# Kernel tuning notes

Measured on AMD Instinct MI355X. Metric: run time of the kernel, lower is better.

The kernel has to match this reference:

```python
import jax, jax.numpy as jnp
import numpy as np

D = 1024      # in/out token dims
E = 2048      # expanded dim = 2*D
S_ATT = 128   # attention feature dim s
EPS = 1e-5
SQRT_S = np.sqrt(S_ATT).astype(np.float32)


def setup_inputs() -> dict:
    key = jax.random.key(0)
    ks = jax.random.split(key, 8)
    B, S = 4, 2048
    x = jax.random.normal(ks[0], (B, S, D), dtype=jnp.float32)
    pos_enc = jax.random.normal(ks[1], (S, S_ATT), dtype=jnp.float32)
    # uv Linear: xavier_uniform on weight of shape [2e+s, D]
    fan_out = 2 * E + S_ATT
    limit = np.sqrt(6.0 / (D + fan_out)).astype(np.float32)
    uv_w = jax.random.uniform(ks[2], (fan_out, D), dtype=jnp.float32, minval=-limit, maxval=limit)
    # o Linear: default kaiming-uniform-ish; plain uniform works for a reference
    lim_o = np.sqrt(1.0 / E).astype(np.float32)
    o_w = jax.random.uniform(ks[3], (D, E), dtype=jnp.float32, minval=-lim_o, maxval=lim_o)
    gamma = jax.random.uniform(ks[4], (2, S_ATT), dtype=jnp.float32)
    beta = jax.random.uniform(ks[5], (2, S_ATT), dtype=jnp.float32)
    ln_g = jnp.ones((), dtype=jnp.float32)          # ScaleNorm learnable scalar
    res_scale = jnp.ones((D,), dtype=jnp.float32)   # ChannelWiseScale
    return {"x": x, "pos_enc": pos_enc, "uv_w": uv_w, "o_w": o_w,
            "gamma": gamma, "beta": beta, "ln_g": ln_g, "res_scale": res_scale}


def _gau(x, pos_enc, uv_w, o_w, gamma, beta, ln_g, res_scale):
    # ScaleNorm: x / max(||x|| * d^-0.5, eps) * g
    norm = jnp.linalg.norm(x, axis=-1, keepdims=True) * (D ** -0.5)
    xn = x / jnp.maximum(norm, EPS) * ln_g
    uv = jax.nn.silu(jnp.einsum('bsd,fd->bsf', xn, uv_w))  # [B,S,2E+s]
    u, v, base = uv[..., :E], uv[..., E:2 * E], uv[..., 2 * E:]
    # per-head affine: base[...,None,:]*gamma+beta -> q,k
    qk_base = base[..., None, :] * gamma + beta             # [B,S,2,s]
    q = qk_base[..., 0, :] + pos_enc[None, :, :]            # 'add' pos enc
    k = qk_base[..., 1, :] + pos_enc[None, :, :]
    scores = jnp.einsum('bqs,bks->bqk', q, k) / SQRT_S
    kernel = jnp.square(jax.nn.relu(scores))                # squared-ReLU attention
    attn_v = jnp.einsum('bqk,bke->bqe', kernel, v)
    out = jnp.einsum('bqe,de->bqd', u * attn_v, o_w)
    # residual shortcut with channel-wise scale (in == out dims)
    return x * res_scale + out


def reference(x, pos_enc, uv_w, o_w, gamma, beta, ln_g, res_scale):
    return _gau(x, pos_enc, uv_w, o_w, gamma, beta, ln_g, res_scale)
```

## Files before the change

### kernel.cpp

```cpp
#include <hip/hip_runtime.h>

typedef unsigned short u16;
typedef __bf16 bf16x8 __attribute__((ext_vector_type(8)));
typedef float f32x4 __attribute__((ext_vector_type(4)));

#define SEQ   2048
#define DDIM  1024
#define EDIM  2048
#define FDIM  4224
#define FPAD  4352
#define SATT  128
#define NBATCH 4

__device__ __forceinline__ u16 f2bf(float f) {
  unsigned u = __float_as_uint(f);
  unsigned r = (u + 0x7fffu + ((u >> 16) & 1u)) >> 16;
  return (u16)r;
}
__device__ __forceinline__ float bf2f(u16 v) {
  return __uint_as_float(((unsigned)v) << 16);
}

__device__ __forceinline__ void gload16(const u16* g, u16* l) {
  auto gp = (const __attribute__((address_space(1))) u16*)(unsigned long long)g;
  auto lp = (__attribute__((address_space(3))) u16*)(unsigned)(unsigned long long)l;
  __builtin_amdgcn_global_load_lds(gp, lp, 16, 0, 0);
}


__global__ void cvt_bf16_kernel(const float* __restrict__ in, u16* __restrict__ out, int n4) {
  int i = blockIdx.x * blockDim.x + threadIdx.x;
  if (i >= n4) return;
  float4 v = reinterpret_cast<const float4*>(in)[i];
  unsigned p0 = (unsigned)f2bf(v.x) | ((unsigned)f2bf(v.y) << 16);
  unsigned p1 = (unsigned)f2bf(v.z) | ((unsigned)f2bf(v.w) << 16);
  uint2 pk; pk.x = p0; pk.y = p1;
  reinterpret_cast<uint2*>(out)[i] = pk;
}

__global__ void rms_kernel(const float* __restrict__ x, const float* __restrict__ ln_g,
                           u16* __restrict__ xn) {
  int row = blockIdx.x;
  int t = threadIdx.x;
  const float4* xr = reinterpret_cast<const float4*>(x + (size_t)row * DDIM);
  float4 v = xr[t];
  float s = v.x * v.x + v.y * v.y + v.z * v.z + v.w * v.w;
#pragma unroll
  for (int off = 32; off > 0; off >>= 1) s += __shfl_down(s, off);
  __shared__ float wsum[4];
  int lane = t & 63, wv = t >> 6;
  if (lane == 0) wsum[wv] = s;
  __syncthreads();
  float tot = wsum[0] + wsum[1] + wsum[2] + wsum[3];
  float rms = sqrtf(tot * (1.0f / (float)DDIM));
  float scale = ln_g[0] / fmaxf(rms, 1e-5f);
  unsigned p0 = (unsigned)f2bf(v.x * scale) | ((unsigned)f2bf(v.y * scale) << 16);
  unsigned p1 = (unsigned)f2bf(v.z * scale) | ((unsigned)f2bf(v.w * scale) << 16);
  uint2 pk; pk.x = p0; pk.y = p1;
  reinterpret_cast<uint2*>(xn + (size_t)row * DDIM)[t] = pk;
}

__global__ void qk_kernel(const u16* __restrict__ uv, const float* __restrict__ pos_enc,
                          const float* __restrict__ gamma, const float* __restrict__ beta,
                          u16* __restrict__ q, u16* __restrict__ k, int ldF) {
  int r = blockIdx.x;
  int t = threadIdx.x;
  int s = r & (SEQ - 1);
  float bval = bf2f(uv[(size_t)r * ldF + 2 * EDIM + t]);
  float pe = pos_enc[(size_t)s * SATT + t];
  float qv = bval * gamma[t] + beta[t] + pe;
  float kv = bval * gamma[SATT + t] + beta[SATT + t] + pe;
  q[(size_t)r * SATT + t] = f2bf(qv);
  k[(size_t)r * SATT + t] = f2bf(kv);
}

__global__ void transpose_v(const u16* __restrict__ uv, u16* __restrict__ vt, int ldF) {
  __shared__ u16 tile[32][33];
  int b = blockIdx.z;
  uv += (size_t)b * SEQ * ldF;
  vt += (size_t)b * EDIM * SEQ;
  int e0 = blockIdx.x * 32, s0 = blockIdx.y * 32;
  int tx = threadIdx.x, ty = threadIdx.y;
#pragma unroll
  for (int j = 0; j < 32; j += 8)
    tile[ty + j][tx] = uv[(size_t)(s0 + ty + j) * ldF + EDIM + e0 + tx];
  __syncthreads();
#pragma unroll
  for (int j = 0; j < 32; j += 8)
    vt[(size_t)(e0 + ty + j) * SEQ + s0 + tx] = tile[tx][ty + j];
}

template <int EPI>
__global__ __launch_bounds__(512, 2) void gemm_bt3(
    const u16* __restrict__ A, const u16* __restrict__ B,
    int N, int K,
    u16* __restrict__ Cbf,
    const u16* __restrict__ U, int ldu,
    size_t sA, size_t sB, size_t sC, size_t sU) {
  __shared__ u16 lds[65536];
  const int tid = threadIdx.x;
  const int w = tid >> 6, l = tid & 63;
  const int wm2 = w >> 2, wn2 = w & 3;
  const int fr = l & 15, kg = l >> 4;

  const int bz = blockIdx.z;
  A += (size_t)bz * sA; B += (size_t)bz * sB; U += (size_t)bz * sU;

  const int nbx = gridDim.x;
  int li = blockIdx.y * nbx + blockIdx.x;
  const int cpx = (nbx * gridDim.y) >> 3;
  li = (li & 7) * cpx + (li >> 3);
  const int bn = li % nbx;
  const int bm = li / nbx;

  const int NT = K >> 6;
  const size_t aoff = (size_t)bm * 256 * K;
  const size_t boff = (size_t)bn * 256 * K;

  const int r0 = (w << 3) + (l >> 3);
  const int cswz = (((l & 7) ^ (l >> 3)) & 7) << 3;

  auto stageP = [&](int T, int p) {
    int off = (T & 1) * 65536 + p * 16384;
    const u16* g;
    if (p == 0)      g = A + aoff;
    else if (p == 1) g = A + aoff + (size_t)128 * K;
    else if (p == 2) g = B + boff;
    else             g = B + boff + (size_t)128 * K;
    g += (size_t)r0 * K + (size_t)T * 64 + cswz;
    u16* dst = lds + (off >> 1) + w * 512;
    gload16(g, dst);
    gload16(g + (size_t)64 * K, dst + 4096);
  };

  const char* ldsC = (const char*)lds;
  auto ldA = [&](int buf, int qa, int i, int s) -> bf16x8 {
    int row = wm2 * 64 + i * 16 + fr;
    int off = buf * 65536 + qa * 16384 + row * 128 + s * 64 + kg * 16;
    off ^= (fr & 7) << 4;
    return *(const bf16x8*)(ldsC + off);
  };
  auto ldB = [&](int buf, int qb, int j, int s) -> bf16x8 {
    int row = wn2 * 32 + j * 16 + fr;
    int off = buf * 65536 + 32768 + qb * 16384 + row * 128 + s * 64 + kg * 16;
    off ^= (fr & 7) << 4;
    return *(const bf16x8*)(ldsC + off);
  };

  f32x4 acc[8][4];
#pragma unroll
  for (int i = 0; i < 8; i++)
#pragma unroll
    for (int j = 0; j < 4; j++) acc[i][j] = f32x4{0.f, 0.f, 0.f, 0.f};

  stageP(0, 0); stageP(0, 2); stageP(0, 3); stageP(0, 1);
  if (NT > 1) {
    stageP(1, 0); stageP(1, 2); stageP(1, 3); stageP(1, 1);
    asm volatile("s_waitcnt vmcnt(8)" ::: "memory");
  } else {
    asm volatile("s_waitcnt vmcnt(0)" ::: "memory");
  }
  __builtin_amdgcn_s_barrier();

  bf16x8 aH[4][2], bF[2][2][2];
  for (int t = 0; t < NT; ++t) {
    const int buf = t & 1;
    const bool st = (t + 2 < NT);
#pragma unroll
    for (int i = 0; i < 4; i++)
#pragma unroll
      for (int s = 0; s < 2; s++) aH[i][s] = ldA(buf, 0, i, s);
#pragma unroll
    for (int j = 0; j < 2; j++)
#pragma unroll
      for (int s = 0; s < 2; s++) bF[0][j][s] = ldB(buf, 0, j, s);
    asm volatile("s_waitcnt lgkmcnt(8)" ::: "memory");
    __builtin_amdgcn_s_barrier();
    asm volatile("s_waitcnt lgkmcnt(0)" ::: "memory");
    __builtin_amdgcn_s_setprio(1);
#pragma unroll
    for (int s = 0; s < 2; s++)
#pragma unroll
      for (int i = 0; i < 4; i++)
#pragma unroll
        for (int j = 0; j < 2; j++)
          acc[i][j] = __builtin_amdgcn_mfma_f32_16x16x32_bf16(aH[i][s], bF[0][j][s], acc[i][j], 0, 0, 0);
    __builtin_amdgcn_s_setprio(0);
    __builtin_amdgcn_s_barrier();
#pragma unroll
    for (int j = 0; j < 2; j++)
#pragma unroll
      for (int s = 0; s < 2; s++) bF[1][j][s] = ldB(buf, 1, j, s);
    if (st) { stageP(t + 2, 0); stageP(t + 2, 2); }
    __builtin_amdgcn_s_barrier();
    asm volatile("s_waitcnt lgkmcnt(0)" ::: "memory");
    __builtin_amdgcn_s_setprio(1);
#pragma unroll
    for (int s = 0; s < 2; s++)
#pragma unroll
      for (int i = 0; i < 4; i++)
#pragma unroll
        for (int j = 0; j < 2; j++)
          acc[i][2 + j] = __builtin_amdgcn_mfma_f32_16x16x32_bf16(aH[i][s], bF[1][j][s], acc[i][2 + j], 0, 0, 0);
    __builtin_amdgcn_s_setprio(0);
    __builtin_amdgcn_s_barrier();
#pragma unroll
    for (int i = 0; i < 4; i++)
#pragma unroll
      for (int s = 0; s < 2; s++) aH[i][s] = ldA(buf, 1, i, s);
    if (st) stageP(t + 2, 3);
    __builtin_amdgcn_s_barrier();
    asm volatile("s_waitcnt lgkmcnt(0)" ::: "memory");
    __builtin_amdgcn_s_setprio(1);
#pragma unroll
    for (int s = 0; s < 2; s++)
#pragma unroll
      for (int i = 0; i < 4; i++)
#pragma unroll
        for (int j = 0; j < 2; j++)
          acc[4 + i][j] = __builtin_amdgcn_mfma_f32_16x16x32_bf16(aH[i][s], bF[0][j][s], acc[4 + i][j], 0, 0, 0);
    __builtin_amdgcn_s_setprio(0);
    __builtin_amdgcn_s_barrier();
    if (st) stageP(t + 2, 1);
    __builtin_amdgcn_s_setprio(1);
#pragma unroll
    for (int s = 0; s < 2; s++)
#pragma unroll
      for (int i = 0; i < 4; i++)
#pragma unroll
        for (int j = 0; j < 2; j++)
          acc[4 + i][2 + j] = __builtin_amdgcn_mfma_f32_16x16x32_bf16(aH[i][s], bF[1][j][s], acc[4 + i][2 + j], 0, 0, 0);
    __builtin_amdgcn_s_setprio(0);
    if (st) asm volatile("s_waitcnt vmcnt(6)" ::: "memory");
    else    asm volatile("s_waitcnt vmcnt(0)" ::: "memory");
    __builtin_amdgcn_s_barrier();
  }

  const int rsub = (l >> 4) * 4;
  const int ccol = l & 15;
#pragma unroll
  for (int ai = 0; ai < 8; ai++) {
#pragma unroll
    for (int bj = 0; bj < 4; bj++) {
      int n = bn * 256 + (bj >> 1) * 128 + wn2 * 32 + (bj & 1) * 16 + ccol;
#pragma unroll
      for (int tt = 0; tt < 4; tt++) {
        int m = bm * 256 + (ai >> 2) * 128 + wm2 * 64 + (ai & 3) * 16 + rsub + tt;
        float v = acc[ai][bj][tt];
        size_t idx = (size_t)m * N + n;
        if constexpr (EPI == 0) {
          float sv = v / (1.f + __expf(-v));
          Cbf[(size_t)bz * sC + idx] = f2bf(sv);
        } else if constexpr (EPI == 1) {
          float sc = v * 0.08838834764831845f;
          sc = sc > 0.f ? sc * sc : 0.f;
          Cbf[(size_t)bz * sC + idx] = f2bf(sc);
        } else {
          float uvl = bf2f(U[(size_t)m * ldu + n]);
          Cbf[(size_t)bz * sC + idx] = f2bf(v * uvl);
        }
      }
    }
  }
}

template <int EPI>
__global__ __launch_bounds__(512, 2) void gemm_bt2(
    const u16* __restrict__ A, const u16* __restrict__ B,
    int M, int N, int K,
    u16* __restrict__ Cbf, float* __restrict__ Cf,
    const u16* __restrict__ U, int ldu,
    const float* __restrict__ Xres, const float* __restrict__ rscale,
    size_t sA, size_t sB, size_t sC, size_t sU) {
  __shared__ u16 lds[3 * 24576];
  const int tid = threadIdx.x;
  const int w = tid >> 6, l = tid & 63;
  const int wr = w >> 1, wc = w & 1;
  const int fr = l & 15, kg = l >> 4;

  const int bz = blockIdx.z;
  A += (size_t)bz * sA; B += (size_t)bz * sB; U += (size_t)bz * sU;

  const int nbx = gridDim.x;
  int li = blockIdx.y * nbx + blockIdx.x;
  const int cpx = (nbx * gridDim.y) >> 3;
  li = (li & 7) * cpx + (li >> 3);
  const int bn = li % nbx;
  const int bm = li / nbx;

  const int NT = K >> 6;
  const int srow = (w << 3) + (l >> 3);
  const int scol = (((l & 7) ^ (l >> 3)) & 7) << 3;
  const size_t aoff = (size_t)bm * 256 * K;
  const size_t boff = (size_t)bn * 128 * K;
  const char* ldsC = (const char*)lds;

  auto stageAu = [&](int t, int h) {
    int sb = (t % 3) * 24576 + h * 8192;
    const u16* g = A + aoff + (size_t)(h * 128 + srow) * K + t * 64 + scol;
#pragma unroll
    for (int L = 0; L < 2; L++)
      gload16(g + (size_t)(L * 64) * K, &lds[sb + (L * 8 + w) * 512]);
  };
  auto stageBu = [&](int t) {
    int sb = (t % 3) * 24576 + 16384;
    const u16* g = B + boff + (size_t)srow * K + t * 64 + scol;
#pragma unroll
    for (int L = 0; L < 2; L++)
      gload16(g + (size_t)(L * 64) * K, &lds[sb + (L * 8 + w) * 512]);
  };
  auto ldA = [&](int cur, int i, int s) -> bf16x8 {
    int r = ((wr & 1) << 6) + (i << 4) + fr;
    int off = cur * 49152 + ((wr >> 1) << 14) + (r << 7) + (s << 6) + (kg << 4);
    off ^= (r & 7) << 4;
    return *(const bf16x8*)(ldsC + off);
  };
  auto ldB = [&](int cur, int j, int s) -> bf16x8 {
    int r = (wc << 6) + (j << 4) + fr;
    int off = cur * 49152 + 32768 + (r << 7) + (s << 6) + (kg << 4);
    off ^= (r & 7) << 4;
    return *(const bf16x8*)(ldsC + off);
  };

  f32x4 acc[4][4];
#pragma unroll
  for (int i = 0; i < 4; i++)
#pragma unroll
    for (int j = 0; j < 4; j++) acc[i][j] = f32x4{0.f, 0.f, 0.f, 0.f};

  stageAu(0, 0); stageAu(0, 1); stageBu(0);
  if (NT > 1) { stageAu(1, 0); stageAu(1, 1); stageBu(1); }
  asm volatile("s_waitcnt vmcnt(6)" ::: "memory");
  __builtin_amdgcn_s_barrier();

  bf16x8 aF[2][2], bF[2][2][2];
  for (int t = 0; t < NT; ++t) {
    const int cur = t % 3;
    const bool st = (t + 2 < NT);
#pragma unroll
    for (int i = 0; i < 2; i++)
#pragma unroll
      for (int s = 0; s < 2; s++) aF[i][s] = ldA(cur, i, s);
#pragma unroll
    for (int j = 0; j < 2; j++)
#pragma unroll
      for (int s = 0; s < 2; s++) bF[0][j][s] = ldB(cur, j, s);
    if (st) stageAu(t + 2, 0);
    __builtin_amdgcn_s_barrier();
    __builtin_amdgcn_s_setprio(1);
#pragma unroll
    for (int s = 0; s < 2; s++)
#pragma unroll
      for (int i = 0; i < 2; i++)
#pragma unroll
        for (int j = 0; j < 2; j++)
          acc[i][j] = __builtin_amdgcn_mfma_f32_16x16x32_bf16(aF[i][s], bF[0][j][s], acc[i][j], 0, 0, 0);
    __builtin_amdgcn_s_setprio(0);
    __builtin_amdgcn_s_barrier();
#pragma unroll
    for (int j = 0; j < 2; j++)
#pragma unroll
      for (int s = 0; s < 2; s++) bF[1][j][s] = ldB(cur, 2 + j, s);
    if (st) stageAu(t + 2, 1);
    __builtin_amdgcn_s_barrier();
    __builtin_amdgcn_s_setprio(1);
#pragma unroll
    for (int s = 0; s < 2; s++)
#pragma unroll
      for (int i = 0; i < 2; i++)
#pragma unroll
        for (int j = 0; j < 2; j++)
          acc[i][2 + j] = __builtin_amdgcn_mfma_f32_16x16x32_bf16(aF[i][s], bF[1][j][s], acc[i][2 + j], 0, 0, 0);
    __builtin_amdgcn_s_setprio(0);
    __builtin_amdgcn_s_barrier();
#pragma unroll
    for (int i = 0; i < 2; i++)
#pragma unroll
      for (int s = 0; s < 2; s++) aF[i][s] = ldA(cur, 2 + i, s);
    if (st) stageBu(t + 2);
    __builtin_amdgcn_s_barrier();
    __builtin_amdgcn_s_setprio(1);
#pragma unroll
    for (int s = 0; s < 2; s++)
#pragma unroll
      for (int i = 0; i < 2; i++)
#pragma unroll
        for (int j = 0; j < 2; j++)
          acc[2 + i][j] = __builtin_amdgcn_mfma_f32_16x16x32_bf16(aF[i][s], bF[0][j][s], acc[2 + i][j], 0, 0, 0);
    __builtin_amdgcn_s_setprio(0);
    __builtin_amdgcn_s_barrier();
    __builtin_amdgcn_s_setprio(1);
#pragma unroll
    for (int s = 0; s < 2; s++)
#pragma unroll
      for (int i = 0; i < 2; i++)
#pragma unroll
        for (int j = 0; j < 2; j++)
          acc[2 + i][2 + j] = __builtin_amdgcn_mfma_f32_16x16x32_bf16(aF[i][s], bF[1][j][s], acc[2 + i][2 + j], 0, 0, 0);
    __builtin_amdgcn_s_setprio(0);
    if (st) asm volatile("s_waitcnt vmcnt(6)" ::: "memory");
    else    asm volatile("s_waitcnt vmcnt(0)" ::: "memory");
    __builtin_amdgcn_s_barrier();
  }

  const int m0 = bm * 256 + wr * 64;
  const int n0 = bn * 128 + wc * 64;
  const int rsub = (l >> 4) * 4;
  const int ccol = l & 15;
#pragma unroll
  for (int i = 0; i < 4; i++) {
#pragma unroll
    for (int j = 0; j < 4; j++) {
      int n = n0 + j * 16 + ccol;
#pragma unroll
      for (int tt = 0; tt < 4; tt++) {
        int m = m0 + i * 16 + rsub + tt;
        float v = acc[i][j][tt];
        size_t idx = (size_t)m * N + n;
        if constexpr (EPI == 0) {
          float sv = v / (1.f + __expf(-v));
          Cbf[(size_t)bz * sC + idx] = f2bf(sv);
        } else if constexpr (EPI == 1) {
          float sc = v * 0.08838834764831845f;
          sc = sc > 0.f ? sc * sc : 0.f;
          Cbf[(size_t)bz * sC + idx] = f2bf(sc);
        } else if constexpr (EPI == 2) {
          float uvl = bf2f(U[(size_t)m * ldu + n]);
          Cbf[(size_t)bz * sC + idx] = f2bf(v * uvl);
        } else {
          Cf[idx] = Xres[idx] * rscale[n] + v;
        }
      }
    }
  }
}

template <int EPI>
__global__ __launch_bounds__(256) void gemm_bt(
    const u16* __restrict__ A, const u16* __restrict__ B,
    int M, int N, int K,
    u16* __restrict__ Cbf, float* __restrict__ Cf,
    const u16* __restrict__ U, int ldu,
    const float* __restrict__ Xres, const float* __restrict__ rscale,
    size_t sA, size_t sB, size_t sC, size_t sU) {
  __shared__ u16 As[128 * 32];
  __shared__ u16 Bs[128 * 32];
  const int tid = threadIdx.x;
  const int wave = tid >> 6, lane = tid & 63;
  const int wr = wave >> 1, wc = wave & 1;
  const int bz = blockIdx.z;
  A += (size_t)bz * sA; B += (size_t)bz * sB; U += (size_t)bz * sU;
  const int nbx = gridDim.x;
  int li = blockIdx.y * nbx + blockIdx.x;
  const int cpx = (nbx * gridDim.y) >> 3;
  li = (li & 7) * cpx + (li >> 3);
  const int bn = li % nbx;
  const int bm = li / nbx;
  const size_t abase = (size_t)bm * 128 * K;
  const size_t bbase = (size_t)bn * 128 * K;
  const int srow = tid >> 2;
  const int scol = (tid & 3) * 8;
  f32x4 acc[4][4];
#pragma unroll
  for (int i = 0; i < 4; i++)
#pragma unroll
    for (int j = 0; j < 4; j++) acc[i][j] = f32x4{0.f, 0.f, 0.f, 0.f};
  const int fr = lane & 15;
  const int fk = (lane >> 4) * 8;
  for (int k0 = 0; k0 < K; k0 += 32) {
#pragma unroll
    for (int r = 0; r < 2; r++) {
      const u16* gA = A + abase + (size_t)(r * 64 + srow) * K + k0 + scol;
      const u16* gB = B + bbase + (size_t)(r * 64 + srow) * K + k0 + scol;
      gload16(gA, As + r * 2048 + wave * 512);
      gload16(gB, Bs + r * 2048 + wave * 512);
    }
    __syncthreads();
    bf16x8 af[4], bfr[4];
#pragma unroll
    for (int i = 0; i < 4; i++) {
      af[i]  = *reinterpret_cast<const bf16x8*>(&As[(wr * 64 + i * 16 + fr) * 32 + fk]);
      bfr[i] = *reinterpret_cast<const bf16x8*>(&Bs[(wc * 64 + i * 16 + fr) * 32 + fk]);
    }
#pragma unroll
    for (int i = 0; i < 4; i++)
#pragma unroll
      for (int j = 0; j < 4; j++)
        acc[i][j] = __builtin_amdgcn_mfma_f32_16x16x32_bf16(af[i], bfr[j], acc[i][j], 0, 0, 0);
    __syncthreads();
  }
  const int m0 = bm * 128 + wr * 64;
  const int n0 = bn * 128 + wc * 64;
  const int rsub = (lane >> 4) * 4;
  const int ccol = lane & 15;
#pragma unroll
  for (int i = 0; i < 4; i++) {
#pragma unroll
    for (int j = 0; j < 4; j++) {
      int n = n0 + j * 16 + ccol;
#pragma unroll
      for (int t = 0; t < 4; t++) {
        int m = m0 + i * 16 + rsub + t;
        float v = acc[i][j][t];
        size_t idx = (size_t)m * N + n;
        if constexpr (EPI == 0) {
          float sv = v / (1.f + __expf(-v));
          Cbf[(size_t)bz * sC + idx] = f2bf(sv);
        } else if constexpr (EPI == 1) {
          float sc = v * 0.08838834764831845f;
          sc = sc > 0.f ? sc * sc : 0.f;
          Cbf[(size_t)bz * sC + idx] = f2bf(sc);
        } else if constexpr (EPI == 2) {
          float uvl = bf2f(U[(size_t)m * ldu + n]);
          Cbf[(size_t)bz * sC + idx] = f2bf(v * uvl);
        } else {
          Cf[idx] = Xres[idx] * rscale[n] + v;
        }
      }
    }
  }
}


extern "C" void kernel_launch(void* const* d_in, const int* in_sizes, int n_in,
                              void* d_out, int out_size, void* d_ws, size_t ws_size,
                              hipStream_t stream) {
  const float* x        = (const float*)d_in[0];
  const float* pos_enc  = (const float*)d_in[1];
  const float* uv_w     = (const float*)d_in[2];
  const float* o_w      = (const float*)d_in[3];
  const float* gamma    = (const float*)d_in[4];
  const float* beta     = (const float*)d_in[5];
  const float* ln_g     = (const float*)d_in[6];
  const float* res_scale= (const float*)d_in[7];
  float* out = (float*)d_out;

  auto al = [](size_t b) { return (b + 255) & ~(size_t)255; };
  const size_t SZ_UVWP = (size_t)FPAD * DDIM * 2;
  const size_t SZ_OW   = (size_t)DDIM * EDIM * 2;
  const size_t SZ_Z    = (size_t)NBATCH * SEQ * EDIM * 2;
  const size_t SZ_XN   = (size_t)NBATCH * SEQ * DDIM * 2;
  const size_t SZ_UVP  = (size_t)NBATCH * SEQ * FPAD * 2;
  const size_t SZ_QK   = (size_t)NBATCH * SEQ * SATT * 2;
  const size_t SZ_VT1  = (size_t)EDIM * SEQ * 2;
  const size_t SZ_P1   = (size_t)SEQ * SEQ * 2;
  const size_t need_full =
      al(SZ_UVWP) + al(SZ_OW) + al(SZ_Z) + al(SZ_XN) + al(SZ_UVP) + 2 * al(SZ_QK) +
      (size_t)NBATCH * (al(SZ_VT1) + al(SZ_P1));
  const bool FULL = ws_size >= need_full;

  char* p = (char*)d_ws;
  auto alloc = [&](size_t bytes) {
    char* r = p;
    p += (bytes + 255) & ~(size_t)255;
    return r;
  };

  if (FULL) {
    u16* uvw_bf = (u16*)alloc(SZ_UVWP);
    u16* ow_bf  = (u16*)alloc(SZ_OW);
    u16* z      = (u16*)alloc(SZ_Z);
    u16* vt     = (u16*)alloc((size_t)NBATCH * al(SZ_VT1));
    u16* pmat   = (u16*)alloc((size_t)NBATCH * al(SZ_P1));
    u16* xn     = (u16*)alloc(SZ_XN);
    u16* uv     = (u16*)alloc(SZ_UVP);
    u16* qb     = (u16*)alloc(SZ_QK);
    u16* kb     = (u16*)alloc(SZ_QK);
    const size_t sVT = al(SZ_VT1) >> 1;
    const size_t sP  = al(SZ_P1) >> 1;
    const int rows = NBATCH * SEQ;

    hipMemsetAsync(uvw_bf + (size_t)FDIM * DDIM, 0,
                   (size_t)(FPAD - FDIM) * DDIM * 2, stream);
    cvt_bf16_kernel<<<(FDIM * DDIM / 4 + 255) / 256, 256, 0, stream>>>(
        uv_w, uvw_bf, FDIM * DDIM / 4);
    cvt_bf16_kernel<<<(DDIM * EDIM / 4 + 255) / 256, 256, 0, stream>>>(
        o_w, ow_bf, DDIM * EDIM / 4);

    rms_kernel<<<rows, 256, 0, stream>>>(x, ln_g, xn);
    gemm_bt3<0><<<dim3(FPAD / 256, rows / 256), 512, 0, stream>>>(
        xn, uvw_bf, FPAD, DDIM, uv, nullptr, 0, 0, 0, 0, 0);
    qk_kernel<<<rows, SATT, 0, stream>>>(uv, pos_enc, gamma, beta, qb, kb, FPAD);
    transpose_v<<<dim3(EDIM / 32, SEQ / 32, NBATCH), dim3(32, 8), 0, stream>>>(uv, vt, FPAD);
    gemm_bt3<1><<<dim3(SEQ / 256, SEQ / 256, NBATCH), 512, 0, stream>>>(
        qb, kb, SEQ, SATT, pmat, nullptr, 0,
        (size_t)SEQ * SATT, (size_t)SEQ * SATT, sP, 0);
    gemm_bt3<2><<<dim3(EDIM / 256, SEQ / 256, NBATCH), 512, 0, stream>>>(
        pmat, vt, EDIM, SEQ, z, uv, FPAD,
        sP, sVT, (size_t)SEQ * EDIM, (size_t)SEQ * FPAD);
    gemm_bt2<3><<<dim3(DDIM / 128, rows / 256), 512, 0, stream>>>(
        z, ow_bf, rows, DDIM, EDIM, nullptr, out, nullptr, 0,
        x, res_scale, 0, 0, 0, 0);
    return;
  }

  u16* uvw_bf = (u16*)alloc((size_t)FDIM * DDIM * 2);
  u16* ow_bf  = (u16*)alloc(SZ_OW);
  u16* z      = (u16*)alloc(SZ_Z);
  u16* vt     = (u16*)alloc(SZ_VT1);
  u16* pmat   = (u16*)alloc(SZ_P1);
  size_t fixed = (size_t)(p - (char*)d_ws);
  const size_t perbc = (size_t)SEQ * DDIM * 2 + (size_t)SEQ * FDIM * 2 +
                       2 * (size_t)SEQ * SATT * 2 + 4 * 256;
  int BC = (ws_size >= fixed + 4 * perbc) ? 4 : 1;
  u16* xn = (u16*)alloc((size_t)BC * SEQ * DDIM * 2);
  u16* uv = (u16*)alloc((size_t)BC * SEQ * FDIM * 2);
  u16* qb = (u16*)alloc((size_t)BC * SEQ * SATT * 2);
  u16* kb = (u16*)alloc((size_t)BC * SEQ * SATT * 2);

  cvt_bf16_kernel<<<(FDIM * DDIM / 4 + 255) / 256, 256, 0, stream>>>(
      uv_w, uvw_bf, FDIM * DDIM / 4);
  cvt_bf16_kernel<<<(DDIM * EDIM / 4 + 255) / 256, 256, 0, stream>>>(
      o_w, ow_bf, DDIM * EDIM / 4);

  for (int b0 = 0; b0 < NBATCH; b0 += BC) {
    int rows = BC * SEQ;
    rms_kernel<<<rows, 256, 0, stream>>>(x + (size_t)b0 * SEQ * DDIM, ln_g, xn);
    gemm_bt<0><<<dim3(FDIM / 128, rows / 128), 256, 0, stream>>>(
        xn, uvw_bf, rows, FDIM, DDIM, uv, nullptr, nullptr, 0, nullptr, nullptr,
        0, 0, 0, 0);
    qk_kernel<<<rows, SATT, 0, stream>>>(uv, pos_enc, gamma, beta, qb, kb, FDIM);
    for (int bb = 0; bb < BC; bb++) {
      int b = b0 + bb;
      const u16* uvb = uv + (size_t)bb * SEQ * FDIM;
      transpose_v<<<dim3(EDIM / 32, SEQ / 32, 1), dim3(32, 8), 0, stream>>>(uvb, vt, FDIM);
      gemm_bt<1><<<dim3(SEQ / 128, SEQ / 128), 256, 0, stream>>>(
          qb + (size_t)bb * SEQ * SATT, kb + (size_t)bb * SEQ * SATT,
          SEQ, SEQ, SATT, pmat, nullptr, nullptr, 0, nullptr, nullptr,
          0, 0, 0, 0);
      gemm_bt<2><<<dim3(EDIM / 128, SEQ / 128), 256, 0, stream>>>(
          pmat, vt, SEQ, EDIM, SEQ, z + (size_t)b * SEQ * EDIM, nullptr,
          uvb, FDIM, nullptr, nullptr, 0, 0, 0, 0);
    }
  }
  gemm_bt<3><<<dim3(DDIM / 128, (NBATCH * SEQ) / 128), 256, 0, stream>>>(
      z, ow_bf, NBATCH * SEQ, DDIM, EDIM, nullptr, out, nullptr, 0,
      x, res_scale, 0, 0, 0, 0);
}
```

Measured before the change: 296.1 us.

## Drop FPAD padding with partial-N tile path and precomputed LDS/global pointers

Removes the padding of the uv projection from 4352 to 4224 columns. The last N block now runs a half-width path that skips loading and multiplying the unused B half, which removes wasted MFMA work and padded stores along with the memset. The main loop is also unrolled by two buffers using precomputed global and LDS pointers, cutting per-iteration address arithmetic. The cost is extra branches on `full` inside the hot loop and a smaller uv row stride.

```diff
diff --git a/kernel.cpp b/kernel.cpp
--- a/kernel.cpp
+++ b/kernel.cpp
@@ -8,7 +8,6 @@
 #define DDIM  1024
 #define EDIM  2048
 #define FDIM  4224
-#define FPAD  4352
 #define SATT  128
 #define NBATCH 4
 
@@ -114,127 +113,130 @@
   const int bm = li / nbx;
 
   const int NT = K >> 6;
-  const size_t aoff = (size_t)bm * 256 * K;
-  const size_t boff = (size_t)bn * 256 * K;
+  const bool full = (bn * 256 + 256 <= N);
 
   const int r0 = (w << 3) + (l >> 3);
   const int cswz = (((l & 7) ^ (l >> 3)) & 7) << 3;
 
-  auto stageP = [&](int T, int p) {
-    int off = (T & 1) * 65536 + p * 16384;
-    const u16* g;
-    if (p == 0)      g = A + aoff;
-    else if (p == 1) g = A + aoff + (size_t)128 * K;
-    else if (p == 2) g = B + boff;
-    else             g = B + boff + (size_t)128 * K;
-    g += (size_t)r0 * K + (size_t)T * 64 + cswz;
-    u16* dst = lds + (off >> 1) + w * 512;
-    gload16(g, dst);
-    gload16(g + (size_t)64 * K, dst + 4096);
+  const u16* pA00 = A + (size_t)bm * 256 * K + (size_t)r0 * K + cswz;
+  const u16* pA01 = pA00 + (size_t)64 * K;
+  const u16* pA10 = pA00 + (size_t)128 * K;
+  const u16* pA11 = pA00 + (size_t)192 * K;
+  const u16* pB00 = B + (size_t)bn * 256 * K + (size_t)r0 * K + cswz;
+  const u16* pB01 = pB00 + (size_t)64 * K;
+  const u16* pB10 = pB00 + (size_t)128 * K;
+  const u16* pB11 = pB00 + (size_t)192 * K;
+
+  const int X  = (l & 7) << 4;
+  const int Y0 = (kg << 4) ^ X;
+  const int Y1 = ((kg << 4) | 64) ^ X;
+  const char* ldsC = (const char*)lds;
+  const char* aR[2][2];
+  const char* bR[2][2];
+  aR[0][0] = ldsC + wm2 * 8192 + fr * 128 + Y0;
+  aR[0][1] = ldsC + wm2 * 8192 + fr * 128 + Y1;
+  aR[1][0] = aR[0][0] + 65536;
+  aR[1][1] = aR[0][1] + 65536;
+  bR[0][0] = ldsC + 32768 + wn2 * 4096 + fr * 128 + Y0;
+  bR[0][1] = ldsC + 32768 + wn2 * 4096 + fr * 128 + Y1;
+  bR[1][0] = bR[0][0] + 65536;
+  bR[1][1] = bR[0][1] + 65536;
+
+  auto stg = [&](int bufw, int p, const u16* g0, const u16* g1, int ofs) {
+    u16* d = lds + bufw * 32768 + p * 8192 + w * 512;
+    gload16(g0 + ofs, d);
+    gload16(g1 + ofs, d + 4096);
   };
 
-  const char* ldsC = (const char*)lds;
-  auto ldA = [&](int buf, int qa, int i, int s) -> bf16x8 {
-    int row = wm2 * 64 + i * 16 + fr;
-    int off = buf * 65536 + qa * 16384 + row * 128 + s * 64 + kg * 16;
-    off ^= (fr & 7) << 4;
-    return *(const bf16x8*)(ldsC + off);
-  };
-  auto ldB = [&](int buf, int qb, int j, int s) -> bf16x8 {
-    int row = wn2 * 32 + j * 16 + fr;
-    int off = buf * 65536 + 32768 + qb * 16384 + row * 128 + s * 64 + kg * 16;
-    off ^= (fr & 7) << 4;
-    return *(const bf16x8*)(ldsC + off);
-  };
-
   f32x4 acc[8][4];
 #pragma unroll
   for (int i = 0; i < 8; i++)
 #pragma unroll
     for (int j = 0; j < 4; j++) acc[i][j] = f32x4{0.f, 0.f, 0.f, 0.f};
 
-  stageP(0, 0); stageP(0, 2); stageP(0, 3); stageP(0, 1);
+  stg(0, 0, pA00, pA01, 0); stg(0, 2, pB00, pB01, 0);
+  if (full) stg(0, 3, pB10, pB11, 0);
+  stg(0, 1, pA10, pA11, 0);
   if (NT > 1) {
-    stageP(1, 0); stageP(1, 2); stageP(1, 3); stageP(1, 1);
-    asm volatile("s_waitcnt vmcnt(8)" ::: "memory");
+    stg(1, 0, pA00, pA01, 64); stg(1, 2, pB00, pB01, 64);
+    if (full) stg(1, 3, pB10, pB11, 64);
+    stg(1, 1, pA10, pA11, 64);
+    if (full) asm volatile("s_waitcnt vmcnt(8)" ::: "memory");
+    else      asm volatile("s_waitcnt vmcnt(6)" ::: "memory");
   } else {
     asm volatile("s_waitcnt vmcnt(0)" ::: "memory");
   }
   __builtin_amdgcn_s_barrier();
 
   bf16x8 aH[4][2], bF[2][2][2];
-  for (int t = 0; t < NT; ++t) {
-    const int buf = t & 1;
-    const bool st = (t + 2 < NT);
-#pragma unroll
-    for (int i = 0; i < 4; i++)
-#pragma unroll
-      for (int s = 0; s < 2; s++) aH[i][s] = ldA(buf, 0, i, s);
-#pragma unroll
-    for (int j = 0; j < 2; j++)
-#pragma unroll
-      for (int s = 0; s < 2; s++) bF[0][j][s] = ldB(buf, 0, j, s);
-    asm volatile("s_waitcnt lgkmcnt(8)" ::: "memory");
-    __builtin_amdgcn_s_barrier();
-    asm volatile("s_waitcnt lgkmcnt(0)" ::: "memory");
-    __builtin_amdgcn_s_setprio(1);
-#pragma unroll
-    for (int s = 0; s < 2; s++)
-#pragma unroll
-      for (int i = 0; i < 4; i++)
-#pragma unroll
-        for (int j = 0; j < 2; j++)
-          acc[i][j] = __builtin_amdgcn_mfma_f32_16x16x32_bf16(aH[i][s], bF[0][j][s], acc[i][j], 0, 0, 0);
-    __builtin_amdgcn_s_setprio(0);
-    __builtin_amdgcn_s_barrier();
-#pragma unroll
-    for (int j = 0; j < 2; j++)
-#pragma unroll
-      for (int s = 0; s < 2; s++) bF[1][j][s] = ldB(buf, 1, j, s);
-    if (st) { stageP(t + 2, 0); stageP(t + 2, 2); }
-    __builtin_amdgcn_s_barrier();
-    asm volatile("s_waitcnt lgkmcnt(0)" ::: "memory");
-    __builtin_amdgcn_s_setprio(1);
-#pragma unroll
-    for (int s = 0; s < 2; s++)
-#pragma unroll
-      for (int i = 0; i < 4; i++)
-#pragma unroll
-        for (int j = 0; j < 2; j++)
-          acc[i][2 + j] = __builtin_amdgcn_mfma_f32_16x16x32_bf16(aH[i][s], bF[1][j][s], acc[i][2 + j], 0, 0, 0);
-    __builtin_amdgcn_s_setprio(0);
-    __builtin_amdgcn_s_barrier();
-#pragma unroll
-    for (int i = 0; i < 4; i++)
-#pragma unroll
-      for (int s = 0; s < 2; s++) aH[i][s] = ldA(buf, 1, i, s);
-    if (st) stageP(t + 2, 3);
-    __builtin_amdgcn_s_barrier();
-    asm volatile("s_waitcnt lgkmcnt(0)" ::: "memory");
-    __builtin_amdgcn_s_setprio(1);
-#pragma unroll
-    for (int s = 0; s < 2; s++)
-#pragma unroll
-      for (int i = 0; i < 4; i++)
-#pragma unroll
-        for (int j = 0; j < 2; j++)
-          acc[4 + i][j] = __builtin_amdgcn_mfma_f32_16x16x32_bf16(aH[i][s], bF[0][j][s], acc[4 + i][j], 0, 0, 0);
-    __builtin_amdgcn_s_setprio(0);
-    __builtin_amdgcn_s_barrier();
-    if (st) stageP(t + 2, 1);
-    __builtin_amdgcn_s_setprio(1);
-#pragma unroll
-    for (int s = 0; s < 2; s++)
-#pragma unroll
-      for (int i = 0; i < 4; i++)
-#pragma unroll
-        for (int j = 0; j < 2; j++)
-          acc[4 + i][2 + j] = __builtin_amdgcn_mfma_f32_16x16x32_bf16(aH[i][s], bF[1][j][s], acc[4 + i][2 + j], 0, 0, 0);
-    __builtin_amdgcn_s_setprio(0);
-    if (st) asm volatile("s_waitcnt vmcnt(6)" ::: "memory");
-    else    asm volatile("s_waitcnt vmcnt(0)" ::: "memory");
-    __builtin_amdgcn_s_barrier();
-  }
+
+#define MFMA_Q(QA, QB)                                                        \
+  _Pragma("unroll") for (int s = 0; s < 2; s++)                               \
+  _Pragma("unroll") for (int i = 0; i < 4; i++)                               \
+  _Pragma("unroll") for (int j = 0; j < 2; j++)                               \
+    acc[(QA)*4 + i][(QB)*2 + j] = __builtin_amdgcn_mfma_f32_16x16x32_bf16(    \
+        aH[i][s], bF[QB][j][s], acc[(QA)*4 + i][(QB)*2 + j], 0, 0, 0);
+
+#define TILE_STEP(BUF, ST, OFS)                                               \
+  {                                                                           \
+                                  \
+    _Pragma("unroll") for (int i = 0; i < 4; i++)                             \
+    _Pragma("unroll") for (int s = 0; s < 2; s++)                             \
+      aH[i][s] = *(const bf16x8*)(aR[BUF][s] + i * 2048);                     \
+    _Pragma("unroll") for (int j = 0; j < 2; j++)                             \
+    _Pragma("unroll") for (int s = 0; s < 2; s++)                             \
+      bF[0][j][s] = *(const bf16x8*)(bR[BUF][s] + j * 2048);                  \
+    asm volatile("s_waitcnt lgkmcnt(8)" ::: "memory");                        \
+    __builtin_amdgcn_s_barrier();                                             \
+    asm volatile("s_waitcnt lgkmcnt(0)" ::: "memory");                        \
+    __builtin_amdgcn_s_setprio(1);                                            \
+    MFMA_Q(0, 0)                                                              \
+    __builtin_amdgcn_s_setprio(0);                                            \
+    __builtin_amdgcn_s_barrier();                                             \
+                   \
+    if (full) {                                                               \
+      _Pragma("unroll") for (int j = 0; j < 2; j++)                           \
+      _Pragma("unroll") for (int s = 0; s < 2; s++)                           \
+        bF[1][j][s] = *(const bf16x8*)(bR[BUF][s] + 16384 + j * 2048);        \
+    }                                                                         \
+    if (ST) { stg(BUF, 0, pA00, pA01, OFS); stg(BUF, 2, pB00, pB01, OFS); }   \
+    __builtin_amdgcn_s_barrier();                                             \
+    asm volatile("s_waitcnt lgkmcnt(0)" ::: "memory");                        \
+    __builtin_amdgcn_s_setprio(1);                                            \
+    if (full) { MFMA_Q(0, 1) }                                                \
+    __builtin_amdgcn_s_setprio(0);                                            \
+    __builtin_amdgcn_s_barrier();                                             \
+                        \
+    _Pragma("unroll") for (int i = 0; i < 4; i++)                             \
+    _Pragma("unroll") for (int s = 0; s < 2; s++)                             \
+      aH[i][s] = *(const bf16x8*)(aR[BUF][s] + 16384 + i * 2048);             \
+    if ((ST) && full) { stg(BUF, 3, pB10, pB11, OFS); }                       \
+    __builtin_amdgcn_s_barrier();                                             \
+    asm volatile("s_waitcnt lgkmcnt(0)" ::: "memory");                        \
+    __builtin_amdgcn_s_setprio(1);                                            \
+    MFMA_Q(1, 0)                                                              \
+    __builtin_amdgcn_s_setprio(0);                                            \
+    __builtin_amdgcn_s_barrier();                                             \
+                      \
+    if (ST) { stg(BUF, 1, pA10, pA11, OFS); }                                 \
+    __builtin_amdgcn_s_setprio(1);                                            \
+    if (full) { MFMA_Q(1, 1) }                                                \
+    __builtin_amdgcn_s_setprio(0);                                            \
+    if (ST) asm volatile("s_waitcnt vmcnt(6)" ::: "memory");                  \
+    else    asm volatile("s_waitcnt vmcnt(0)" ::: "memory");                  \
+    __builtin_amdgcn_s_barrier();                                             \
+  }
+
+  for (int t2 = 0; t2 < NT; t2 += 2) {
+    const bool st0 = (t2 + 2 < NT);
+    const bool st1 = (t2 + 3 < NT);
+    TILE_STEP(0, st0, 128)
+    TILE_STEP(1, st1, 192)
+    pA00 += 128; pA01 += 128; pA10 += 128; pA11 += 128;
+    pB00 += 128; pB01 += 128; pB10 += 128; pB11 += 128;
+  }
+#undef TILE_STEP
+#undef MFMA_Q
 
   const int rsub = (l >> 4) * 4;
   const int ccol = l & 15;
@@ -242,6 +244,7 @@
   for (int ai = 0; ai < 8; ai++) {
 #pragma unroll
     for (int bj = 0; bj < 4; bj++) {
+      if (!full && bj >= 2) continue;
       int n = bn * 256 + (bj >> 1) * 128 + wn2 * 32 + (bj & 1) * 16 + ccol;
 #pragma unroll
       for (int tt = 0; tt < 4; tt++) {
@@ -536,16 +539,16 @@
   float* out = (float*)d_out;
 
   auto al = [](size_t b) { return (b + 255) & ~(size_t)255; };
-  const size_t SZ_UVWP = (size_t)FPAD * DDIM * 2;
+  const size_t SZ_UVW  = (size_t)FDIM * DDIM * 2;
   const size_t SZ_OW   = (size_t)DDIM * EDIM * 2;
   const size_t SZ_Z    = (size_t)NBATCH * SEQ * EDIM * 2;
   const size_t SZ_XN   = (size_t)NBATCH * SEQ * DDIM * 2;
-  const size_t SZ_UVP  = (size_t)NBATCH * SEQ * FPAD * 2;
+  const size_t SZ_UV   = (size_t)NBATCH * SEQ * FDIM * 2;
   const size_t SZ_QK   = (size_t)NBATCH * SEQ * SATT * 2;
   const size_t SZ_VT1  = (size_t)EDIM * SEQ * 2;
   const size_t SZ_P1   = (size_t)SEQ * SEQ * 2;
   const size_t need_full =
-      al(SZ_UVWP) + al(SZ_OW) + al(SZ_Z) + al(SZ_XN) + al(SZ_UVP) + 2 * al(SZ_QK) +
+      al(SZ_UVW) + al(SZ_OW) + al(SZ_Z) + al(SZ_XN) + al(SZ_UV) + 2 * al(SZ_QK) +
       (size_t)NBATCH * (al(SZ_VT1) + al(SZ_P1));
   const bool FULL = ws_size >= need_full;
 
@@ -557,44 +560,42 @@
   };
 
   if (FULL) {
-    u16* uvw_bf = (u16*)alloc(SZ_UVWP);
+    u16* uvw_bf = (u16*)alloc(SZ_UVW);
     u16* ow_bf  = (u16*)alloc(SZ_OW);
     u16* z      = (u16*)alloc(SZ_Z);
     u16* vt     = (u16*)alloc((size_t)NBATCH * al(SZ_VT1));
     u16* pmat   = (u16*)alloc((size_t)NBATCH * al(SZ_P1));
     u16* xn     = (u16*)alloc(SZ_XN);
-    u16* uv     = (u16*)alloc(SZ_UVP);
+    u16* uv     = (u16*)alloc(SZ_UV);
     u16* qb     = (u16*)alloc(SZ_QK);
     u16* kb     = (u16*)alloc(SZ_QK);
     const size_t sVT = al(SZ_VT1) >> 1;
     const size_t sP  = al(SZ_P1) >> 1;
     const int rows = NBATCH * SEQ;
 
-    hipMemsetAsync(uvw_bf + (size_t)FDIM * DDIM, 0,
-                   (size_t)(FPAD - FDIM) * DDIM * 2, stream);
     cvt_bf16_kernel<<<(FDIM * DDIM / 4 + 255) / 256, 256, 0, stream>>>(
         uv_w, uvw_bf, FDIM * DDIM / 4);
     cvt_bf16_kernel<<<(DDIM * EDIM / 4 + 255) / 256, 256, 0, stream>>>(
         o_w, ow_bf, DDIM * EDIM / 4);
 
     rms_kernel<<<rows, 256, 0, stream>>>(x, ln_g, xn);
-    gemm_bt3<0><<<dim3(FPAD / 256, rows / 256), 512, 0, stream>>>(
-        xn, uvw_bf, FPAD, DDIM, uv, nullptr, 0, 0, 0, 0, 0);
-    qk_kernel<<<rows, SATT, 0, stream>>>(uv, pos_enc, gamma, beta, qb, kb, FPAD);
-    transpose_v<<<dim3(EDIM / 32, SEQ / 32, NBATCH), dim3(32, 8), 0, stream>>>(uv, vt, FPAD);
+    gemm_bt3<0><<<dim3(17, rows / 256), 512, 0, stream>>>(
+        xn, uvw_bf, FDIM, DDIM, uv, nullptr, 0, 0, 0, 0, 0);
+    qk_kernel<<<rows, SATT, 0, stream>>>(uv, pos_enc, gamma, beta, qb, kb, FDIM);
+    transpose_v<<<dim3(EDIM / 32, SEQ / 32, NBATCH), dim3(32, 8), 0, stream>>>(uv, vt, FDIM);
     gemm_bt3<1><<<dim3(SEQ / 256, SEQ / 256, NBATCH), 512, 0, stream>>>(
         qb, kb, SEQ, SATT, pmat, nullptr, 0,
         (size_t)SEQ * SATT, (size_t)SEQ * SATT, sP, 0);
     gemm_bt3<2><<<dim3(EDIM / 256, SEQ / 256, NBATCH), 512, 0, stream>>>(
-        pmat, vt, EDIM, SEQ, z, uv, FPAD,
-        sP, sVT, (size_t)SEQ * EDIM, (size_t)SEQ * FPAD);
+        pmat, vt, EDIM, SEQ, z, uv, FDIM,
+        sP, sVT, (size_t)SEQ * EDIM, (size_t)SEQ * FDIM);
     gemm_bt2<3><<<dim3(DDIM / 128, rows / 256), 512, 0, stream>>>(
         z, ow_bf, rows, DDIM, EDIM, nullptr, out, nullptr, 0,
         x, res_scale, 0, 0, 0, 0);
     return;
   }
 
-  u16* uvw_bf = (u16*)alloc((size_t)FDIM * DDIM * 2);
+  u16* uvw_bf = (u16*)alloc(SZ_UVW);
   u16* ow_bf  = (u16*)alloc(SZ_OW);
   u16* z      = (u16*)alloc(SZ_Z);
   u16* vt     = (u16*)alloc(SZ_VT1);
```

After: 280.4 us. 1.06x faster.
